# Optimization experiments

Hardware: AMD Instinct MI355X
Metric: run time of the kernel (lower is better)

Reference implementation:

```python
import jax, jax.numpy as jnp
import numpy as np

Np_, Ny, Nu = 5, 8, 4
NZ = Np_ * (Ny + Nu)  # 60


def setup_inputs() -> dict:
    key = jax.random.key(0)
    ks = jax.random.split(key, 6)
    B, T = 8192, 1024
    u = jax.random.normal(ks[0], (B, T, Nu), dtype=jnp.float32)
    z0 = jax.random.normal(ks[1], (B, NZ), dtype=jnp.float32)
    W1 = jax.random.normal(ks[2], (NZ, 128), dtype=jnp.float32) * (1.0 / np.sqrt(NZ))
    b1 = jnp.zeros((128,), dtype=jnp.float32)
    W2 = jax.random.normal(ks[3], (128, 128), dtype=jnp.float32) * (1.0 / np.sqrt(128))
    b2 = jnp.zeros((128,), dtype=jnp.float32)
    W3 = jax.random.normal(ks[4], (128, Ny), dtype=jnp.float32) * (1.0 / np.sqrt(128))
    b3 = jnp.zeros((Ny,), dtype=jnp.float32)
    return {"u": u, "z0": z0, "W1": W1, "b1": b1, "W2": W2, "b2": b2,
            "W3": W3, "b3": b3}


def reference(u, z0, W1, b1, W2, b2, W3, b3):
    # u: [B, T, Nu], z0: [B, Np*(Ny+Nu)] -> y sequence [B, T, Ny]
    def step(z, u_t):
        h = jnp.tanh(z @ W1 + b1)
        h = jnp.tanh(h @ W2 + b2)
        y = h @ W3 + b3                      # [B, Ny]
        ypseq = z[:, : Np_ * Ny]
        upseq = z[:, Np_ * Ny:]
        z_new = jnp.concatenate(
            (ypseq[:, Ny:], y, upseq[:, Nu:], u_t), axis=-1)
        return z_new, y

    u_tbc = jnp.transpose(u, (1, 0, 2))      # [T, B, Nu]
    _, ys = jax.lax.scan(step, z0, u_tbc)    # ys: [T, B, Ny]
    return jnp.transpose(ys, (1, 0, 2))      # [B, T, Ny]
```

## Files before the change

### kernel.cpp

```cpp
#include <hip/hip_runtime.h>

#define T_STEPS 1024
#define NZV 60
#define H 128
#define NY 8
#define NU 4
#define ZSTR 72
#define HSTR 136
#define YBSTR 132

typedef __attribute__((ext_vector_type(8))) short bf16x8;
typedef __attribute__((ext_vector_type(4))) short bf16x4;
typedef __attribute__((ext_vector_type(4))) float f32x4;
typedef __attribute__((ext_vector_type(2))) unsigned uint2v;

union U4 { unsigned u[4]; bf16x8 v; };
union U2 { unsigned u[2]; bf16x4 v; };

__device__ __forceinline__ unsigned short f2bf(float x) {
    unsigned u = __float_as_uint(x);
    u += 0x7FFFu + ((u >> 16) & 1u);
    return (unsigned short)(u >> 16);
}

__device__ __forceinline__ unsigned cvt_pk_bf16(float lo, float hi) {
    unsigned r;
    asm("v_cvt_pk_bf16_f32 %0, %1, %2" : "=v"(r) : "v"(lo), "v"(hi));
    return r;
}

__device__ __forceinline__ unsigned swz16(unsigned v) {
    return (unsigned)__builtin_amdgcn_ds_swizzle((int)v, 0x401F);
}

__device__ __forceinline__ float tanh_fast(float x) {
    float e = __builtin_amdgcn_exp2f(x * 2.8853900817779268f);
    return fmaf(-2.0f, __builtin_amdgcn_rcpf(e + 1.0f), 1.0f);
}

#define MFMA32 __builtin_amdgcn_mfma_f32_16x16x32_bf16

__device__ __forceinline__ f32x4 gemm3_pair(bf16x4 a0, bf16x4 b0,
                                            bf16x4 a1, bf16x4 b1, f32x4 c) {
    asm("s_nop 1\n\t"
        "v_mfma_f32_16x16x16_bf16 %0, %1, %2, %0\n\t"
        "v_mfma_f32_16x16x16_bf16 %0, %3, %4, %0\n\t"
        "s_nop 7\n\t"
        "s_nop 7"
        : "+v"(c) : "v"(a0), "v"(b0), "v"(a1), "v"(b1));
    return c;
}

__global__ __launch_bounds__(256, 2)
void cstr_scan_kernel(const float* __restrict__ u_g, const float* __restrict__ z0_g,
                      const float* __restrict__ W1, const float* __restrict__ b1,
                      const float* __restrict__ W2, const float* __restrict__ b2,
                      const float* __restrict__ W3, const float* __restrict__ b3,
                      float* __restrict__ out) {
    __shared__ unsigned short zbuf[2][16][ZSTR];
    __shared__ unsigned short h1s[16][HSTR];
    __shared__ f32x4 ypart[4][72];
    __shared__ float ybuf[32 * YBSTR];
    __shared__ float ubuf[2][16][16][NU];

    const int tid   = threadIdx.x;
    const int wid   = tid >> 6;
    const int lane  = tid & 63;
    const int b0    = blockIdx.x * 16;
    const int col   = lane & 15;
    const int kg    = lane >> 4;
    const int urow  = lane >> 2;
    const int uc    = lane & 3;
    const int nbase = wid * 32;
    const int frow  = tid >> 4;
    const int ftoff = tid & 15;
    const int ypIdx = lane + (lane >> 3);

    bf16x8 w1f[2][2], w2f[4][2];
    bf16x4 w3a0, w3a1;
    f32x4 b1t[2], b2t[2], b3t;
#pragma unroll
    for (int nl = 0; nl < 2; ++nl)
#pragma unroll
        for (int r = 0; r < 4; ++r) {
            b1t[nl][r] = b1[nbase + nl * 16 + kg * 4 + r];
            b2t[nl][r] = b2[nbase + nl * 16 + kg * 4 + r];
        }
#pragma unroll
    for (int r = 0; r < 4; ++r) {
        int m = kg * 4 + r;
        b3t[r] = (m < NY) ? b3[m] : 0.f;
    }
#pragma unroll
    for (int kc = 0; kc < 2; ++kc)
#pragma unroll
        for (int nl = 0; nl < 2; ++nl) {
            bf16x8 v;
#pragma unroll
            for (int j = 0; j < 8; ++j) {
                int k = kc * 32 + kg * 8 + j;
                float w = (k < NZV) ? W1[k * H + nbase + nl * 16 + col] : 0.f;
                v[j] = (short)f2bf(w);
            }
            w1f[kc][nl] = v;
        }
#pragma unroll
    for (int kc = 0; kc < 4; ++kc)
#pragma unroll
        for (int nl = 0; nl < 2; ++nl) {
            bf16x8 v;
#pragma unroll
            for (int j = 0; j < 8; ++j) {
                int k = kc * 32 + kg * 8 + j;
                v[j] = (short)f2bf(W2[k * H + nbase + nl * 16 + col]);
            }
            w2f[kc][nl] = v;
        }
    {
        bf16x4 v0, v1;
#pragma unroll
        for (int j = 0; j < 4; ++j) {
            v0[j] = (short)f2bf((col < NY) ? W3[(nbase + 0  + kg * 4 + j) * NY + col] : 0.f);
            v1[j] = (short)f2bf((col < NY) ? W3[(nbase + 16 + kg * 4 + j) * NY + col] : 0.f);
        }
        w3a0 = v0; w3a1 = v1;
    }

#define LOAD_UWIN(BI, T0)                                                              \
    if (wid == 1) {                                                                    \
        const float* usrc = u_g + (size_t)(b0 + (lane & 15)) * (T_STEPS * NU)          \
                            + (size_t)((T0) + (lane >> 4)) * NU;                       \
        _Pragma("unroll")                                                              \
        for (int k_ = 0; k_ < 4; ++k_)                                                 \
            __builtin_amdgcn_global_load_lds(                                          \
                (const __attribute__((address_space(1))) unsigned*)(usrc + k_ * 16),   \
                (__attribute__((address_space(3))) unsigned*)(&ubuf[BI][k_ * 4][0][0]),\
                16, 0, 0);                                                             \
    }

    {
        unsigned short* zs = &zbuf[0][0][0];
        for (int i = tid; i < 2 * 16 * ZSTR; i += 256) zs[i] = 0;
        __syncthreads();
        for (int i = tid; i < 16 * NZV; i += 256) {
            int r = i / NZV, c = i - r * NZV;
            zbuf[0][r][c] = f2bf(z0_g[(size_t)(b0 + r) * NZV + c]);
        }
        LOAD_UWIN(0, 0)
        __syncthreads();
    }

    bf16x8 za0, za1l;
    int t = 0;

    {
        bf16x8 pza0 = *(const bf16x8*)&zbuf[0][col][kg * 8];
        bf16x8 pza1 = *(const bf16x8*)&zbuf[0][col][32 + kg * 8];
#pragma unroll
        for (int nl = 0; nl < 2; ++nl) {
            f32x4 c1 = b1t[nl];
            c1 = MFMA32(w1f[0][nl], pza0, c1, 0, 0, 0);
            c1 = MFMA32(w1f[1][nl], pza1, c1, 0, 0, 0);
            unsigned p01 = cvt_pk_bf16(tanh_fast(c1[0]), tanh_fast(c1[1]));
            unsigned p23 = cvt_pk_bf16(tanh_fast(c1[2]), tanh_fast(c1[3]));
            *(uint2v*)&h1s[col][nbase + nl * 16 + kg * 4] = uint2v{p01, p23};
        }
        if (wid == 3) {
            bf16x4 m0 = *(const bf16x4*)&zbuf[0][urow][8 + 8 * uc];
            bf16x4 m1 = *(const bf16x4*)&zbuf[0][urow][12 + 8 * uc];
            bf16x4 m2 = *(const bf16x4*)&zbuf[0][urow][44 + 4 * uc];
            *(bf16x4*)&zbuf[1][urow][8 * uc]      = m0;
            *(bf16x4*)&zbuf[1][urow][8 * uc + 4]  = m1;
            *(bf16x4*)&zbuf[1][urow][40 + 4 * uc] = m2;
            zbuf[1][urow][56 + uc] = f2bf(ubuf[0][0][urow][uc]);
        }
        __syncthreads();
        bf16x8 ha0 = *(const bf16x8*)&h1s[col][0 * 32 + kg * 8];
        bf16x8 ha1 = *(const bf16x8*)&h1s[col][1 * 32 + kg * 8];
        bf16x8 ha2 = *(const bf16x8*)&h1s[col][2 * 32 + kg * 8];
        bf16x8 ha3 = *(const bf16x8*)&h1s[col][3 * 32 + kg * 8];
        za0  = *(const bf16x8*)&zbuf[1][col][kg * 8];
        za1l = *(const bf16x8*)&zbuf[1][col][32 + kg * 8];
        bf16x4 pb0, pb1;
#pragma unroll
        for (int nl = 0; nl < 2; ++nl) {
            f32x4 a0 = b2t[nl];
            f32x4 a1 = { 0.f, 0.f, 0.f, 0.f };
            a0 = MFMA32(w2f[0][nl], ha0, a0, 0, 0, 0);
            a1 = MFMA32(w2f[1][nl], ha1, a1, 0, 0, 0);
            a0 = MFMA32(w2f[2][nl], ha2, a0, 0, 0, 0);
            a1 = MFMA32(w2f[3][nl], ha3, a1, 0, 0, 0);
            f32x4 c2 = a0 + a1;
            U2 p; p.u[0] = cvt_pk_bf16(tanh_fast(c2[0]), tanh_fast(c2[1]));
            p.u[1]       = cvt_pk_bf16(tanh_fast(c2[2]), tanh_fast(c2[3]));
            if (nl == 0) pb0 = p.v; else pb1 = p.v;
        }
        f32x4 yp = (wid == 0) ? b3t : f32x4{0.f, 0.f, 0.f, 0.f};
        yp = gemm3_pair(w3a0, pb0, w3a1, pb1, yp);
        ypart[wid][ypIdx] = yp;
        __syncthreads();
        t = 1;
    }

#define BODY(P)                                                                         \
    {                                                                                   \
                  \
        f32x4 y_ = ypart[0][ypIdx] + ypart[1][ypIdx] + ypart[2][ypIdx] + ypart[3][ypIdx];\
        unsigned d0 = cvt_pk_bf16(y_[0], y_[1]);                                        \
        unsigned d1 = cvt_pk_bf16(y_[2], y_[3]);                                        \
        unsigned o0 = swz16(d0);                                                        \
        unsigned o1 = swz16(d1);                                                        \
        U4 zb_; zb_.u[0] = d0; zb_.u[1] = d1; zb_.u[2] = o0; zb_.u[3] = o1;             \
        bf16x8 za1 = (kg == 0) ? zb_.v : za1l;      \
        if (wid == 1 && kg < 2) {                                                       \
            *(f32x4*)&ybuf[((t - 1) & 31) * YBSTR + col * 8 + kg * 4] = y_;             \
            *(uint2v*)&zbuf[(P) ^ 1][col][24 + kg * 4] = uint2v{d0, d1};                \
        }                                                                               \
        _Pragma("unroll")                                                               \
        for (int nl = 0; nl < 2; ++nl) {                                                \
            f32x4 c1 = b1t[nl];                                                         \
            c1 = MFMA32(w1f[0][nl], za0, c1, 0, 0, 0);                                  \
            c1 = MFMA32(w1f[1][nl], za1, c1, 0, 0, 0);                                  \
            unsigned p01 = cvt_pk_bf16(tanh_fast(c1[0]), tanh_fast(c1[1]));             \
            unsigned p23 = cvt_pk_bf16(tanh_fast(c1[2]), tanh_fast(c1[3]));             \
            *(uint2v*)&h1s[col][nbase + nl * 16 + kg * 4] = uint2v{p01, p23};           \
        }                                                                               \
        if (wid == 3) {    \
            if (uc < 3) {                                                               \
                bf16x4 m0 = *(const bf16x4*)&zbuf[P][urow][8 + 8 * uc];                 \
                bf16x4 m1 = *(const bf16x4*)&zbuf[P][urow][12 + 8 * uc];                \
                *(bf16x4*)&zbuf[(P) ^ 1][urow][8 * uc]     = m0;                        \
                *(bf16x4*)&zbuf[(P) ^ 1][urow][8 * uc + 4] = m1;                        \
            }                                                                           \
            bf16x4 m2 = *(const bf16x4*)&zbuf[P][urow][44 + 4 * uc];                    \
            *(bf16x4*)&zbuf[(P) ^ 1][urow][40 + 4 * uc] = m2;                           \
            zbuf[(P) ^ 1][urow][56 + uc] = f2bf(ubuf[(t >> 4) & 1][t & 15][urow][uc]);  \
        }                                                                               \
        __syncthreads();                          \
        bf16x8 ha0 = *(const bf16x8*)&h1s[col][0 * 32 + kg * 8];                        \
        bf16x8 ha1 = *(const bf16x8*)&h1s[col][1 * 32 + kg * 8];                        \
        bf16x8 ha2 = *(const bf16x8*)&h1s[col][2 * 32 + kg * 8];                        \
        bf16x8 ha3 = *(const bf16x8*)&h1s[col][3 * 32 + kg * 8];                        \
        za0  = *(const bf16x8*)&zbuf[(P) ^ 1][col][kg * 8];            \
        za1l = *(const bf16x8*)&zbuf[(P) ^ 1][col][32 + kg * 8];                        \
        __builtin_amdgcn_s_setprio(1);                                                  \
        bf16x4 pb0, pb1;                                                                \
        _Pragma("unroll")                                                               \
        for (int nl = 0; nl < 2; ++nl) {                                                \
            f32x4 a0 = b2t[nl];                                                         \
            f32x4 a1 = { 0.f, 0.f, 0.f, 0.f };                                          \
            a0 = MFMA32(w2f[0][nl], ha0, a0, 0, 0, 0);                                  \
            a1 = MFMA32(w2f[1][nl], ha1, a1, 0, 0, 0);                                  \
            a0 = MFMA32(w2f[2][nl], ha2, a0, 0, 0, 0);                                  \
            a1 = MFMA32(w2f[3][nl], ha3, a1, 0, 0, 0);                                  \
            f32x4 c2 = a0 + a1;                                                         \
            U2 p; p.u[0] = cvt_pk_bf16(tanh_fast(c2[0]), tanh_fast(c2[1]));             \
            p.u[1]       = cvt_pk_bf16(tanh_fast(c2[2]), tanh_fast(c2[3]));             \
            if (nl == 0) pb0 = p.v; else pb1 = p.v;                                     \
        }                                                                               \
        f32x4 yp = (wid == 0) ? b3t : f32x4{0.f, 0.f, 0.f, 0.f};                        \
        yp = gemm3_pair(w3a0, pb0, w3a1, pb1, yp);                                      \
        __builtin_amdgcn_s_setprio(0);                                                  \
        ypart[wid][ypIdx] = yp;                                                         \
        __syncthreads();                             \
        ++t;                                                                            \
    }

#define FLUSH(BT)                                                                       \
    {                                                                                   \
        const f32x4* yp_ = (const f32x4*)&ybuf[(((BT) & 31) + ftoff) * YBSTR + frow * 8];\
        f32x4 v0 = yp_[0], v1 = yp_[1];                                                 \
        float* op = out + ((size_t)(b0 + frow) * T_STEPS + (BT) + ftoff) * NY;          \
        *(f32x4*)op = v0;                                                               \
        *(f32x4*)(op + 4) = v1;                                                         \
    }

#pragma unroll 1
    for (int it = 0; it < 511; ++it) {
        if ((t & 15) == 1) {
            if (t > 1)
                FLUSH(t - 17)
            if (t + 15 < T_STEPS)
                LOAD_UWIN((((t + 15) >> 4) & 1), t + 15)
        }
        BODY(1)
        BODY(0)
    }
    BODY(1)
#undef BODY

    {
        if (wid == 1 && kg < 2) {
            f32x4 y_ = ypart[0][ypIdx] + ypart[1][ypIdx] + ypart[2][ypIdx] + ypart[3][ypIdx];
            *(f32x4*)&ybuf[31 * YBSTR + col * 8 + kg * 4] = y_;
        }
        __syncthreads();
        const f32x4* yp_ = (const f32x4*)&ybuf[(16 + ftoff) * YBSTR + frow * 8];
        f32x4 v0 = yp_[0], v1 = yp_[1];
        float* op = out + ((size_t)(b0 + frow) * T_STEPS + 1008 + ftoff) * NY;
        *(f32x4*)op = v0;
        *(f32x4*)(op + 4) = v1;
    }
#undef FLUSH
#undef LOAD_UWIN
}

extern "C" void kernel_launch(void* const* d_in, const int* in_sizes, int n_in,
                              void* d_out, int out_size, void* d_ws, size_t ws_size,
                              hipStream_t stream) {
    (void)in_sizes; (void)n_in; (void)d_ws; (void)ws_size; (void)out_size;
    const float* u  = (const float*)d_in[0];
    const float* z0 = (const float*)d_in[1];
    const float* W1 = (const float*)d_in[2];
    const float* b1 = (const float*)d_in[3];
    const float* W2 = (const float*)d_in[4];
    const float* b2 = (const float*)d_in[5];
    const float* W3 = (const float*)d_in[6];
    const float* b3 = (const float*)d_in[7];
    float* out = (float*)d_out;

    dim3 grid(8192 / 16);
    dim3 block(256);
    cstr_scan_kernel<<<grid, block, 0, stream>>>(u, z0, W1, b1, W2, b2, W3, b3, out);
}
```

Measured before the change: 940.8 us.

## Process two independent 16-row batch tiles per block to interleave recurrences

Each block now handles 32 batch rows as two independent 16-row recurrences (A and B), interleaving their MFMA and tanh work within one barrier per step. This halves the grid to 256 blocks and lowers launch bounds to one block per SIMD group. The u window prefetch through global_load_lds is replaced by per-step scalar register prefetch in two waves. The aim is to hide the serial dependency latency of each step with independent work while amortising barriers, at the cost of fewer blocks, lower occupancy and possibly poor CU coverage on a 256-CU device.

```diff
diff --git a/kernel.cpp b/kernel.cpp
--- a/kernel.cpp
+++ b/kernel.cpp
@@ -51,22 +51,21 @@
     return c;
 }
 
-__global__ __launch_bounds__(256, 2)
+__global__ __launch_bounds__(256, 1)
 void cstr_scan_kernel(const float* __restrict__ u_g, const float* __restrict__ z0_g,
                       const float* __restrict__ W1, const float* __restrict__ b1,
                       const float* __restrict__ W2, const float* __restrict__ b2,
                       const float* __restrict__ W3, const float* __restrict__ b3,
                       float* __restrict__ out) {
-    __shared__ unsigned short zbuf[2][16][ZSTR];
-    __shared__ unsigned short h1s[16][HSTR];
-    __shared__ f32x4 ypart[4][72];
-    __shared__ float ybuf[32 * YBSTR];
-    __shared__ float ubuf[2][16][16][NU];
+    __shared__ unsigned short zbuf[2][2][16][ZSTR];
+    __shared__ unsigned short h1s[2][16][HSTR];
+    __shared__ f32x4 ypart[2][4][72];
+    __shared__ float ybuf[2][32 * YBSTR];
 
     const int tid   = threadIdx.x;
     const int wid   = tid >> 6;
     const int lane  = tid & 63;
-    const int b0    = blockIdx.x * 16;
+    const int b0    = blockIdx.x * 32;
     const int col   = lane & 15;
     const int kg    = lane >> 4;
     const int urow  = lane >> 2;
@@ -126,163 +125,263 @@
         w3a0 = v0; w3a1 = v1;
     }
 
-#define LOAD_UWIN(BI, T0)                                                              \
-    if (wid == 1) {                                                                    \
-        const float* usrc = u_g + (size_t)(b0 + (lane & 15)) * (T_STEPS * NU)          \
-                            + (size_t)((T0) + (lane >> 4)) * NU;                       \
-        _Pragma("unroll")                                                              \
-        for (int k_ = 0; k_ < 4; ++k_)                                                 \
-            __builtin_amdgcn_global_load_lds(                                          \
-                (const __attribute__((address_space(1))) unsigned*)(usrc + k_ * 16),   \
-                (__attribute__((address_space(3))) unsigned*)(&ubuf[BI][k_ * 4][0][0]),\
-                16, 0, 0);                                                             \
-    }
-
     {
-        unsigned short* zs = &zbuf[0][0][0];
-        for (int i = tid; i < 2 * 16 * ZSTR; i += 256) zs[i] = 0;
+        unsigned short* zs = &zbuf[0][0][0][0];
+        for (int i = tid; i < 2 * 2 * 16 * ZSTR; i += 256) zs[i] = 0;
         __syncthreads();
-        for (int i = tid; i < 16 * NZV; i += 256) {
+        for (int i = tid; i < 32 * NZV; i += 256) {
             int r = i / NZV, c = i - r * NZV;
-            zbuf[0][r][c] = f2bf(z0_g[(size_t)(b0 + r) * NZV + c]);
-        }
-        LOAD_UWIN(0, 0)
+            zbuf[r >> 4][0][r & 15][c] = f2bf(z0_g[(size_t)(b0 + r) * NZV + c]);
+        }
         __syncthreads();
     }
 
-    bf16x8 za0, za1l;
+    const float* uptrA = u_g + (size_t)(b0 + urow) * (T_STEPS * NU) + uc;
+    const float* uptrB = u_g + (size_t)(b0 + 16 + urow) * (T_STEPS * NU) + uc;
+    float uregA = 0.f, uregA_n = 0.f, uregB = 0.f, uregB_n = 0.f;
+    if (wid == 3) uregA = *uptrA;
+    if (wid == 2) uregB = *uptrB;
+
+    bf16x8 za0A, za1lA, za0B, za1lB;
     int t = 0;
 
     {
-        bf16x8 pza0 = *(const bf16x8*)&zbuf[0][col][kg * 8];
-        bf16x8 pza1 = *(const bf16x8*)&zbuf[0][col][32 + kg * 8];
+        bf16x8 pzaA0 = *(const bf16x8*)&zbuf[0][0][col][kg * 8];
+        bf16x8 pzaA1 = *(const bf16x8*)&zbuf[0][0][col][32 + kg * 8];
+        bf16x8 pzaB0 = *(const bf16x8*)&zbuf[1][0][col][kg * 8];
+        bf16x8 pzaB1 = *(const bf16x8*)&zbuf[1][0][col][32 + kg * 8];
 #pragma unroll
         for (int nl = 0; nl < 2; ++nl) {
             f32x4 c1 = b1t[nl];
-            c1 = MFMA32(w1f[0][nl], pza0, c1, 0, 0, 0);
-            c1 = MFMA32(w1f[1][nl], pza1, c1, 0, 0, 0);
+            c1 = MFMA32(w1f[0][nl], pzaA0, c1, 0, 0, 0);
+            c1 = MFMA32(w1f[1][nl], pzaA1, c1, 0, 0, 0);
             unsigned p01 = cvt_pk_bf16(tanh_fast(c1[0]), tanh_fast(c1[1]));
             unsigned p23 = cvt_pk_bf16(tanh_fast(c1[2]), tanh_fast(c1[3]));
-            *(uint2v*)&h1s[col][nbase + nl * 16 + kg * 4] = uint2v{p01, p23};
+            *(uint2v*)&h1s[0][col][nbase + nl * 16 + kg * 4] = uint2v{p01, p23};
+        }
+#pragma unroll
+        for (int nl = 0; nl < 2; ++nl) {
+            f32x4 c1 = b1t[nl];
+            c1 = MFMA32(w1f[0][nl], pzaB0, c1, 0, 0, 0);
+            c1 = MFMA32(w1f[1][nl], pzaB1, c1, 0, 0, 0);
+            unsigned p01 = cvt_pk_bf16(tanh_fast(c1[0]), tanh_fast(c1[1]));
+            unsigned p23 = cvt_pk_bf16(tanh_fast(c1[2]), tanh_fast(c1[3]));
+            *(uint2v*)&h1s[1][col][nbase + nl * 16 + kg * 4] = uint2v{p01, p23};
         }
         if (wid == 3) {
-            bf16x4 m0 = *(const bf16x4*)&zbuf[0][urow][8 + 8 * uc];
-            bf16x4 m1 = *(const bf16x4*)&zbuf[0][urow][12 + 8 * uc];
-            bf16x4 m2 = *(const bf16x4*)&zbuf[0][urow][44 + 4 * uc];
-            *(bf16x4*)&zbuf[1][urow][8 * uc]      = m0;
-            *(bf16x4*)&zbuf[1][urow][8 * uc + 4]  = m1;
-            *(bf16x4*)&zbuf[1][urow][40 + 4 * uc] = m2;
-            zbuf[1][urow][56 + uc] = f2bf(ubuf[0][0][urow][uc]);
+            bf16x4 m0 = *(const bf16x4*)&zbuf[0][0][urow][8 + 8 * uc];
+            bf16x4 m1 = *(const bf16x4*)&zbuf[0][0][urow][12 + 8 * uc];
+            bf16x4 m2 = *(const bf16x4*)&zbuf[0][0][urow][44 + 4 * uc];
+            *(bf16x4*)&zbuf[0][1][urow][8 * uc]      = m0;
+            *(bf16x4*)&zbuf[0][1][urow][8 * uc + 4]  = m1;
+            *(bf16x4*)&zbuf[0][1][urow][40 + 4 * uc] = m2;
+            zbuf[0][1][urow][56 + uc] = f2bf(uregA);
+            uptrA += NU;
+            uregA_n = *uptrA;
+        }
+        if (wid == 2) {
+            bf16x4 m0 = *(const bf16x4*)&zbuf[1][0][urow][8 + 8 * uc];
+            bf16x4 m1 = *(const bf16x4*)&zbuf[1][0][urow][12 + 8 * uc];
+            bf16x4 m2 = *(const bf16x4*)&zbuf[1][0][urow][44 + 4 * uc];
+            *(bf16x4*)&zbuf[1][1][urow][8 * uc]      = m0;
+            *(bf16x4*)&zbuf[1][1][urow][8 * uc + 4]  = m1;
+            *(bf16x4*)&zbuf[1][1][urow][40 + 4 * uc] = m2;
+            zbuf[1][1][urow][56 + uc] = f2bf(uregB);
+            uptrB += NU;
+            uregB_n = *uptrB;
         }
         __syncthreads();
-        bf16x8 ha0 = *(const bf16x8*)&h1s[col][0 * 32 + kg * 8];
-        bf16x8 ha1 = *(const bf16x8*)&h1s[col][1 * 32 + kg * 8];
-        bf16x8 ha2 = *(const bf16x8*)&h1s[col][2 * 32 + kg * 8];
-        bf16x8 ha3 = *(const bf16x8*)&h1s[col][3 * 32 + kg * 8];
-        za0  = *(const bf16x8*)&zbuf[1][col][kg * 8];
-        za1l = *(const bf16x8*)&zbuf[1][col][32 + kg * 8];
+        bf16x8 haA0 = *(const bf16x8*)&h1s[0][col][0 * 32 + kg * 8];
+        bf16x8 haA1 = *(const bf16x8*)&h1s[0][col][1 * 32 + kg * 8];
+        bf16x8 haA2 = *(const bf16x8*)&h1s[0][col][2 * 32 + kg * 8];
+        bf16x8 haA3 = *(const bf16x8*)&h1s[0][col][3 * 32 + kg * 8];
+        bf16x8 haB0 = *(const bf16x8*)&h1s[1][col][0 * 32 + kg * 8];
+        bf16x8 haB1 = *(const bf16x8*)&h1s[1][col][1 * 32 + kg * 8];
+        bf16x8 haB2 = *(const bf16x8*)&h1s[1][col][2 * 32 + kg * 8];
+        bf16x8 haB3 = *(const bf16x8*)&h1s[1][col][3 * 32 + kg * 8];
+        za0A  = *(const bf16x8*)&zbuf[0][1][col][kg * 8];
+        za1lA = *(const bf16x8*)&zbuf[0][1][col][32 + kg * 8];
+        za0B  = *(const bf16x8*)&zbuf[1][1][col][kg * 8];
+        za1lB = *(const bf16x8*)&zbuf[1][1][col][32 + kg * 8];
         bf16x4 pb0, pb1;
 #pragma unroll
         for (int nl = 0; nl < 2; ++nl) {
             f32x4 a0 = b2t[nl];
             f32x4 a1 = { 0.f, 0.f, 0.f, 0.f };
-            a0 = MFMA32(w2f[0][nl], ha0, a0, 0, 0, 0);
-            a1 = MFMA32(w2f[1][nl], ha1, a1, 0, 0, 0);
-            a0 = MFMA32(w2f[2][nl], ha2, a0, 0, 0, 0);
-            a1 = MFMA32(w2f[3][nl], ha3, a1, 0, 0, 0);
+            a0 = MFMA32(w2f[0][nl], haA0, a0, 0, 0, 0);
+            a1 = MFMA32(w2f[1][nl], haA1, a1, 0, 0, 0);
+            a0 = MFMA32(w2f[2][nl], haA2, a0, 0, 0, 0);
+            a1 = MFMA32(w2f[3][nl], haA3, a1, 0, 0, 0);
             f32x4 c2 = a0 + a1;
             U2 p; p.u[0] = cvt_pk_bf16(tanh_fast(c2[0]), tanh_fast(c2[1]));
             p.u[1]       = cvt_pk_bf16(tanh_fast(c2[2]), tanh_fast(c2[3]));
             if (nl == 0) pb0 = p.v; else pb1 = p.v;
         }
-        f32x4 yp = (wid == 0) ? b3t : f32x4{0.f, 0.f, 0.f, 0.f};
-        yp = gemm3_pair(w3a0, pb0, w3a1, pb1, yp);
-        ypart[wid][ypIdx] = yp;
+        f32x4 ypA = (wid == 0) ? b3t : f32x4{0.f, 0.f, 0.f, 0.f};
+        ypA = gemm3_pair(w3a0, pb0, w3a1, pb1, ypA);
+        ypart[0][wid][ypIdx] = ypA;
+#pragma unroll
+        for (int nl = 0; nl < 2; ++nl) {
+            f32x4 a0 = b2t[nl];
+            f32x4 a1 = { 0.f, 0.f, 0.f, 0.f };
+            a0 = MFMA32(w2f[0][nl], haB0, a0, 0, 0, 0);
+            a1 = MFMA32(w2f[1][nl], haB1, a1, 0, 0, 0);
+            a0 = MFMA32(w2f[2][nl], haB2, a0, 0, 0, 0);
+            a1 = MFMA32(w2f[3][nl], haB3, a1, 0, 0, 0);
+            f32x4 c2 = a0 + a1;
+            U2 p; p.u[0] = cvt_pk_bf16(tanh_fast(c2[0]), tanh_fast(c2[1]));
+            p.u[1]       = cvt_pk_bf16(tanh_fast(c2[2]), tanh_fast(c2[3]));
+            if (nl == 0) pb0 = p.v; else pb1 = p.v;
+        }
+        f32x4 ypB = (wid == 0) ? b3t : f32x4{0.f, 0.f, 0.f, 0.f};
+        ypB = gemm3_pair(w3a0, pb0, w3a1, pb1, ypB);
+        ypart[1][wid][ypIdx] = ypB;
         __syncthreads();
+        uregA = uregA_n;
+        uregB = uregB_n;
         t = 1;
     }
 
 #define BODY(P)                                                                         \
     {                                                                                   \
-                  \
-        f32x4 y_ = ypart[0][ypIdx] + ypart[1][ypIdx] + ypart[2][ypIdx] + ypart[3][ypIdx];\
-        unsigned d0 = cvt_pk_bf16(y_[0], y_[1]);                                        \
-        unsigned d1 = cvt_pk_bf16(y_[2], y_[3]);                                        \
-        unsigned o0 = swz16(d0);                                                        \
-        unsigned o1 = swz16(d1);                                                        \
-        U4 zb_; zb_.u[0] = d0; zb_.u[1] = d1; zb_.u[2] = o0; zb_.u[3] = o1;             \
-        bf16x8 za1 = (kg == 0) ? zb_.v : za1l;      \
+        f32x4 yA = ypart[0][0][ypIdx] + ypart[0][1][ypIdx]                              \
+                 + ypart[0][2][ypIdx] + ypart[0][3][ypIdx];                             \
+        f32x4 yB = ypart[1][0][ypIdx] + ypart[1][1][ypIdx]                              \
+                 + ypart[1][2][ypIdx] + ypart[1][3][ypIdx];                             \
+        unsigned dA0 = cvt_pk_bf16(yA[0], yA[1]);                                       \
+        unsigned dA1 = cvt_pk_bf16(yA[2], yA[3]);                                       \
+        unsigned dB0 = cvt_pk_bf16(yB[0], yB[1]);                                       \
+        unsigned dB1 = cvt_pk_bf16(yB[2], yB[3]);                                       \
+        unsigned oA0 = swz16(dA0), oA1 = swz16(dA1);                                    \
+        unsigned oB0 = swz16(dB0), oB1 = swz16(dB1);                                    \
+        U4 zbA; zbA.u[0] = dA0; zbA.u[1] = dA1; zbA.u[2] = oA0; zbA.u[3] = oA1;         \
+        U4 zbB; zbB.u[0] = dB0; zbB.u[1] = dB1; zbB.u[2] = oB0; zbB.u[3] = oB1;         \
+        bf16x8 za1A = (kg == 0) ? zbA.v : za1lA;                                        \
+        bf16x8 za1B = (kg == 0) ? zbB.v : za1lB;                                        \
         if (wid == 1 && kg < 2) {                                                       \
-            *(f32x4*)&ybuf[((t - 1) & 31) * YBSTR + col * 8 + kg * 4] = y_;             \
-            *(uint2v*)&zbuf[(P) ^ 1][col][24 + kg * 4] = uint2v{d0, d1};                \
+            *(f32x4*)&ybuf[0][((t - 1) & 31) * YBSTR + col * 8 + kg * 4] = yA;          \
+            *(uint2v*)&zbuf[0][(P) ^ 1][col][24 + kg * 4] = uint2v{dA0, dA1};           \
+        }                                                                               \
+        if (wid == 0 && kg < 2) {                                                       \
+            *(f32x4*)&ybuf[1][((t - 1) & 31) * YBSTR + col * 8 + kg * 4] = yB;          \
+            *(uint2v*)&zbuf[1][(P) ^ 1][col][24 + kg * 4] = uint2v{dB0, dB1};           \
         }                                                                               \
         _Pragma("unroll")                                                               \
         for (int nl = 0; nl < 2; ++nl) {                                                \
             f32x4 c1 = b1t[nl];                                                         \
-            c1 = MFMA32(w1f[0][nl], za0, c1, 0, 0, 0);                                  \
-            c1 = MFMA32(w1f[1][nl], za1, c1, 0, 0, 0);                                  \
+            c1 = MFMA32(w1f[0][nl], za0A, c1, 0, 0, 0);                                 \
+            c1 = MFMA32(w1f[1][nl], za1A, c1, 0, 0, 0);                                 \
             unsigned p01 = cvt_pk_bf16(tanh_fast(c1[0]), tanh_fast(c1[1]));             \
             unsigned p23 = cvt_pk_bf16(tanh_fast(c1[2]), tanh_fast(c1[3]));             \
-            *(uint2v*)&h1s[col][nbase + nl * 16 + kg * 4] = uint2v{p01, p23};           \
-        }                                                                               \
-        if (wid == 3) {    \
+            *(uint2v*)&h1s[0][col][nbase + nl * 16 + kg * 4] = uint2v{p01, p23};        \
+        }                                                                               \
+        _Pragma("unroll")                                                               \
+        for (int nl = 0; nl < 2; ++nl) {                                                \
+            f32x4 c1 = b1t[nl];                                                         \
+            c1 = MFMA32(w1f[0][nl], za0B, c1, 0, 0, 0);                                 \
+            c1 = MFMA32(w1f[1][nl], za1B, c1, 0, 0, 0);                                 \
+            unsigned p01 = cvt_pk_bf16(tanh_fast(c1[0]), tanh_fast(c1[1]));             \
+            unsigned p23 = cvt_pk_bf16(tanh_fast(c1[2]), tanh_fast(c1[3]));             \
+            *(uint2v*)&h1s[1][col][nbase + nl * 16 + kg * 4] = uint2v{p01, p23};        \
+        }                                                                               \
+        if (wid == 3) {                       \
             if (uc < 3) {                                                               \
-                bf16x4 m0 = *(const bf16x4*)&zbuf[P][urow][8 + 8 * uc];                 \
-                bf16x4 m1 = *(const bf16x4*)&zbuf[P][urow][12 + 8 * uc];                \
-                *(bf16x4*)&zbuf[(P) ^ 1][urow][8 * uc]     = m0;                        \
-                *(bf16x4*)&zbuf[(P) ^ 1][urow][8 * uc + 4] = m1;                        \
+                bf16x4 m0 = *(const bf16x4*)&zbuf[0][P][urow][8 + 8 * uc];              \
+                bf16x4 m1 = *(const bf16x4*)&zbuf[0][P][urow][12 + 8 * uc];             \
+                *(bf16x4*)&zbuf[0][(P) ^ 1][urow][8 * uc]     = m0;                     \
+                *(bf16x4*)&zbuf[0][(P) ^ 1][urow][8 * uc + 4] = m1;                     \
             }                                                                           \
-            bf16x4 m2 = *(const bf16x4*)&zbuf[P][urow][44 + 4 * uc];                    \
-            *(bf16x4*)&zbuf[(P) ^ 1][urow][40 + 4 * uc] = m2;                           \
-            zbuf[(P) ^ 1][urow][56 + uc] = f2bf(ubuf[(t >> 4) & 1][t & 15][urow][uc]);  \
-        }                                                                               \
-        __syncthreads();                          \
-        bf16x8 ha0 = *(const bf16x8*)&h1s[col][0 * 32 + kg * 8];                        \
-        bf16x8 ha1 = *(const bf16x8*)&h1s[col][1 * 32 + kg * 8];                        \
-        bf16x8 ha2 = *(const bf16x8*)&h1s[col][2 * 32 + kg * 8];                        \
-        bf16x8 ha3 = *(const bf16x8*)&h1s[col][3 * 32 + kg * 8];                        \
-        za0  = *(const bf16x8*)&zbuf[(P) ^ 1][col][kg * 8];            \
-        za1l = *(const bf16x8*)&zbuf[(P) ^ 1][col][32 + kg * 8];                        \
+            bf16x4 m2 = *(const bf16x4*)&zbuf[0][P][urow][44 + 4 * uc];                 \
+            *(bf16x4*)&zbuf[0][(P) ^ 1][urow][40 + 4 * uc] = m2;                        \
+            zbuf[0][(P) ^ 1][urow][56 + uc] = f2bf(uregA);                              \
+            uptrA += NU;                                                                \
+            if (t + 1 < T_STEPS) uregA_n = *uptrA;                                      \
+        }                                                                               \
+        if (wid == 2) {                       \
+            if (uc < 3) {                                                               \
+                bf16x4 m0 = *(const bf16x4*)&zbuf[1][P][urow][8 + 8 * uc];              \
+                bf16x4 m1 = *(const bf16x4*)&zbuf[1][P][urow][12 + 8 * uc];             \
+                *(bf16x4*)&zbuf[1][(P) ^ 1][urow][8 * uc]     = m0;                     \
+                *(bf16x4*)&zbuf[1][(P) ^ 1][urow][8 * uc + 4] = m1;                     \
+            }                                                                           \
+            bf16x4 m2 = *(const bf16x4*)&zbuf[1][P][urow][44 + 4 * uc];                 \
+            *(bf16x4*)&zbuf[1][(P) ^ 1][urow][40 + 4 * uc] = m2;                        \
+            zbuf[1][(P) ^ 1][urow][56 + uc] = f2bf(uregB);                              \
+            uptrB += NU;                                                                \
+            if (t + 1 < T_STEPS) uregB_n = *uptrB;                                      \
+        }                                                                               \
+        __syncthreads();                                                        \
+        bf16x8 haA0 = *(const bf16x8*)&h1s[0][col][0 * 32 + kg * 8];                    \
+        bf16x8 haA1 = *(const bf16x8*)&h1s[0][col][1 * 32 + kg * 8];                    \
+        bf16x8 haA2 = *(const bf16x8*)&h1s[0][col][2 * 32 + kg * 8];                    \
+        bf16x8 haA3 = *(const bf16x8*)&h1s[0][col][3 * 32 + kg * 8];                    \
+        bf16x8 haB0 = *(const bf16x8*)&h1s[1][col][0 * 32 + kg * 8];                    \
+        bf16x8 haB1 = *(const bf16x8*)&h1s[1][col][1 * 32 + kg * 8];                    \
+        bf16x8 haB2 = *(const bf16x8*)&h1s[1][col][2 * 32 + kg * 8];                    \
+        bf16x8 haB3 = *(const bf16x8*)&h1s[1][col][3 * 32 + kg * 8];                    \
+        za0A  = *(const bf16x8*)&zbuf[0][(P) ^ 1][col][kg * 8];                         \
+        za1lA = *(const bf16x8*)&zbuf[0][(P) ^ 1][col][32 + kg * 8];                    \
+        za0B  = *(const bf16x8*)&zbuf[1][(P) ^ 1][col][kg * 8];                         \
+        za1lB = *(const bf16x8*)&zbuf[1][(P) ^ 1][col][32 + kg * 8];                    \
         __builtin_amdgcn_s_setprio(1);                                                  \
-        bf16x4 pb0, pb1;                                                                \
+        bf16x4 pbA0, pbA1, pbB0, pbB1;                                                  \
         _Pragma("unroll")                                                               \
         for (int nl = 0; nl < 2; ++nl) {                                                \
             f32x4 a0 = b2t[nl];                                                         \
             f32x4 a1 = { 0.f, 0.f, 0.f, 0.f };                                          \
-            a0 = MFMA32(w2f[0][nl], ha0, a0, 0, 0, 0);                                  \
-            a1 = MFMA32(w2f[1][nl], ha1, a1, 0, 0, 0);                                  \
-            a0 = MFMA32(w2f[2][nl], ha2, a0, 0, 0, 0);                                  \
-            a1 = MFMA32(w2f[3][nl], ha3, a1, 0, 0, 0);                                  \
+            a0 = MFMA32(w2f[0][nl], haA0, a0, 0, 0, 0);                                 \
+            a1 = MFMA32(w2f[1][nl], haA1, a1, 0, 0, 0);                                 \
+            a0 = MFMA32(w2f[2][nl], haA2, a0, 0, 0, 0);                                 \
+            a1 = MFMA32(w2f[3][nl], haA3, a1, 0, 0, 0);                                 \
             f32x4 c2 = a0 + a1;                                                         \
             U2 p; p.u[0] = cvt_pk_bf16(tanh_fast(c2[0]), tanh_fast(c2[1]));             \
             p.u[1]       = cvt_pk_bf16(tanh_fast(c2[2]), tanh_fast(c2[3]));             \
-            if (nl == 0) pb0 = p.v; else pb1 = p.v;                                     \
-        }                                                                               \
-        f32x4 yp = (wid == 0) ? b3t : f32x4{0.f, 0.f, 0.f, 0.f};                        \
-        yp = gemm3_pair(w3a0, pb0, w3a1, pb1, yp);                                      \
+            if (nl == 0) pbA0 = p.v; else pbA1 = p.v;                                   \
+        }                                                                               \
+        _Pragma("unroll")                                                               \
+        for (int nl = 0; nl < 2; ++nl) {                                                \
+            f32x4 a0 = b2t[nl];                                                         \
+            f32x4 a1 = { 0.f, 0.f, 0.f, 0.f };                                          \
+            a0 = MFMA32(w2f[0][nl], haB0, a0, 0, 0, 0);                                 \
+            a1 = MFMA32(w2f[1][nl], haB1, a1, 0, 0, 0);                                 \
+            a0 = MFMA32(w2f[2][nl], haB2, a0, 0, 0, 0);                                 \
+            a1 = MFMA32(w2f[3][nl], haB3, a1, 0, 0, 0);                                 \
+            f32x4 c2 = a0 + a1;                                                         \
+            U2 p; p.u[0] = cvt_pk_bf16(tanh_fast(c2[0]), tanh_fast(c2[1]));             \
+            p.u[1]       = cvt_pk_bf16(tanh_fast(c2[2]), tanh_fast(c2[3]));             \
+            if (nl == 0) pbB0 = p.v; else pbB1 = p.v;                                   \
+        }                                                                               \
+        f32x4 ypA = (wid == 0) ? b3t : f32x4{0.f, 0.f, 0.f, 0.f};                       \
+        ypA = gemm3_pair(w3a0, pbA0, w3a1, pbA1, ypA);                                  \
+        f32x4 ypB = (wid == 0) ? b3t : f32x4{0.f, 0.f, 0.f, 0.f};                       \
+        ypB = gemm3_pair(w3a0, pbB0, w3a1, pbB1, ypB);                                  \
         __builtin_amdgcn_s_setprio(0);                                                  \
-        ypart[wid][ypIdx] = yp;                                                         \
-        __syncthreads();                             \
+        ypart[0][wid][ypIdx] = ypA;                                                     \
+        ypart[1][wid][ypIdx] = ypB;                                                     \
+        __syncthreads();                                                        \
+        uregA = uregA_n;                                                                \
+        uregB = uregB_n;                                                                \
         ++t;                                                                            \
     }
 
 #define FLUSH(BT)                                                                       \
     {                                                                                   \
-        const f32x4* yp_ = (const f32x4*)&ybuf[(((BT) & 31) + ftoff) * YBSTR + frow * 8];\
-        f32x4 v0 = yp_[0], v1 = yp_[1];                                                 \
-        float* op = out + ((size_t)(b0 + frow) * T_STEPS + (BT) + ftoff) * NY;          \
-        *(f32x4*)op = v0;                                                               \
-        *(f32x4*)(op + 4) = v1;                                                         \
+        const f32x4* fpA = (const f32x4*)&ybuf[0][(((BT) & 31) + ftoff) * YBSTR + frow * 8]; \
+        f32x4 fA0 = fpA[0], fA1 = fpA[1];                                               \
+        float* opA = out + ((size_t)(b0 + frow) * T_STEPS + (BT) + ftoff) * NY;         \
+        *(f32x4*)opA = fA0;                                                             \
+        *(f32x4*)(opA + 4) = fA1;                                                       \
+        const f32x4* fpB = (const f32x4*)&ybuf[1][(((BT) & 31) + ftoff) * YBSTR + frow * 8]; \
+        f32x4 fB0 = fpB[0], fB1 = fpB[1];                                               \
+        float* opB = out + ((size_t)(b0 + 16 + frow) * T_STEPS + (BT) + ftoff) * NY;    \
+        *(f32x4*)opB = fB0;                                                             \
+        *(f32x4*)(opB + 4) = fB1;                                                       \
     }
 
 #pragma unroll 1
     for (int it = 0; it < 511; ++it) {
-        if ((t & 15) == 1) {
-            if (t > 1)
-                FLUSH(t - 17)
-            if (t + 15 < T_STEPS)
-                LOAD_UWIN((((t + 15) >> 4) & 1), t + 15)
-        }
+        if ((t & 15) == 1 && t > 1)
+            FLUSH(t - 17)
         BODY(1)
         BODY(0)
     }
@@ -291,18 +390,28 @@
 
     {
         if (wid == 1 && kg < 2) {
-            f32x4 y_ = ypart[0][ypIdx] + ypart[1][ypIdx] + ypart[2][ypIdx] + ypart[3][ypIdx];
-            *(f32x4*)&ybuf[31 * YBSTR + col * 8 + kg * 4] = y_;
+            f32x4 yA = ypart[0][0][ypIdx] + ypart[0][1][ypIdx]
+                     + ypart[0][2][ypIdx] + ypart[0][3][ypIdx];
+            *(f32x4*)&ybuf[0][31 * YBSTR + col * 8 + kg * 4] = yA;
+        }
+        if (wid == 0 && kg < 2) {
+            f32x4 yB = ypart[1][0][ypIdx] + ypart[1][1][ypIdx]
+                     + ypart[1][2][ypIdx] + ypart[1][3][ypIdx];
+            *(f32x4*)&ybuf[1][31 * YBSTR + col * 8 + kg * 4] = yB;
         }
         __syncthreads();
-        const f32x4* yp_ = (const f32x4*)&ybuf[(16 + ftoff) * YBSTR + frow * 8];
-        f32x4 v0 = yp_[0], v1 = yp_[1];
-        float* op = out + ((size_t)(b0 + frow) * T_STEPS + 1008 + ftoff) * NY;
-        *(f32x4*)op = v0;
-        *(f32x4*)(op + 4) = v1;
+        const f32x4* fpA = (const f32x4*)&ybuf[0][(16 + ftoff) * YBSTR + frow * 8];
+        f32x4 fA0 = fpA[0], fA1 = fpA[1];
+        float* opA = out + ((size_t)(b0 + frow) * T_STEPS + 1008 + ftoff) * NY;
+        *(f32x4*)opA = fA0;
+        *(f32x4*)(opA + 4) = fA1;
+        const f32x4* fpB = (const f32x4*)&ybuf[1][(16 + ftoff) * YBSTR + frow * 8];
+        f32x4 fB0 = fpB[0], fB1 = fpB[1];
+        float* opB = out + ((size_t)(b0 + 16 + frow) * T_STEPS + 1008 + ftoff) * NY;
+        *(f32x4*)opB = fB0;
+        *(f32x4*)(opB + 4) = fB1;
     }
 #undef FLUSH
-#undef LOAD_UWIN
 }
 
 extern "C" void kernel_launch(void* const* d_in, const int* in_sizes, int n_in,
@@ -319,7 +428,7 @@
     const float* b3 = (const float*)d_in[7];
     float* out = (float*)d_out;
 
-    dim3 grid(8192 / 16);
+    dim3 grid(8192 / 32);
     dim3 block(256);
     cstr_scan_kernel<<<grid, block, 0, stream>>>(u, z0, W1, b1, W2, b2, W3, b3, out);
 }
```

Measured after the change: 1.413 ms. 50.2% more time.
